# Optimization experiments

Hardware: AMD Instinct MI355X
Metric: run time of the kernel (lower is better)

## Reference

```python
import jax, jax.numpy as jnp
import numpy as np

HEADS = 16
D_MODEL = 1024
HEAD_DIM = D_MODEL // HEADS


def setup_inputs() -> dict:
    key = jax.random.key(0)
    ks = jax.random.split(key, 11)
    B, S = 4, 2048
    scale_in = 1.0 / np.sqrt(HEAD_DIM)
    scale_out = 1.0 / np.sqrt(D_MODEL)
    return {
        "values": jax.random.normal(ks[0], (B, S, D_MODEL), dtype=jnp.float32),
        "keys": jax.random.normal(ks[1], (B, S, D_MODEL), dtype=jnp.float32),
        "query": jax.random.normal(ks[2], (B, S, D_MODEL), dtype=jnp.float32),
        "wq": jax.random.normal(ks[3], (HEAD_DIM, HEAD_DIM), dtype=jnp.float32) * scale_in,
        "bq": jax.random.normal(ks[4], (HEAD_DIM,), dtype=jnp.float32) * 0.01,
        "wk": jax.random.normal(ks[5], (HEAD_DIM, HEAD_DIM), dtype=jnp.float32) * scale_in,
        "bk": jax.random.normal(ks[6], (HEAD_DIM,), dtype=jnp.float32) * 0.01,
        "wv": jax.random.normal(ks[7], (HEAD_DIM, HEAD_DIM), dtype=jnp.float32) * scale_in,
        "bv": jax.random.normal(ks[8], (HEAD_DIM,), dtype=jnp.float32) * 0.01,
        "wo": jax.random.normal(ks[9], (D_MODEL, D_MODEL), dtype=jnp.float32) * scale_out,
        "bo": jax.random.normal(ks[10], (D_MODEL,), dtype=jnp.float32) * 0.01,
    }


def reference(values, keys, query, wq, bq, wk, bk, wv, bv, wo, bo):
    B, Sq = query.shape[0], query.shape[1]
    Sk, Sv = keys.shape[1], values.shape[1]
    # reshape to (n, s, h, d); per-head linear shares one [d,d] weight across heads
    v = values.reshape(B, Sv, HEADS, HEAD_DIM) @ wv.T + bv
    k = keys.reshape(B, Sk, HEADS, HEAD_DIM) @ wk.T + bk
    q = query.reshape(B, Sq, HEADS, HEAD_DIM) @ wq.T + bq
    # scores scaled by sqrt(d_model) (as in original, NOT sqrt(head_dim))
    energy = jnp.einsum("nqhd,nkhd->nhqk", q, k)
    attn = jax.nn.softmax(energy / jnp.sqrt(jnp.float32(D_MODEL)), axis=-1)
    out = jnp.einsum("nhqk,nkhd->nqhd", attn, v).reshape(B, Sq, D_MODEL)
    return out @ wo.T + bo
```

## Files before the change

kernel.cpp:

```cpp
#include <hip/hip_runtime.h>

typedef unsigned short u16;
typedef short  bfrag  __attribute__((ext_vector_type(8), may_alias));
typedef unsigned long long ull_a __attribute__((may_alias));
typedef int    int_a  __attribute__((may_alias));
typedef int    i4_a   __attribute__((ext_vector_type(4), may_alias));
typedef float  f4_a   __attribute__((ext_vector_type(4), may_alias));
typedef unsigned u32x2 __attribute__((ext_vector_type(2)));
typedef __attribute__((ext_vector_type(4)))  float facc4;
typedef __attribute__((ext_vector_type(16))) float facc16;

#define SEQ   2048
#define NHEAD 16
#define HD    64
#define DM    1024
#define BH    64
#define NTOK  8192
#define QSC   0.04508422f

#if defined(__has_builtin)
#if __has_builtin(__builtin_amdgcn_cvt_pk_bf16_f32)
#define HAS_CVT_PK 1
#endif
#if __has_builtin(__builtin_amdgcn_permlane32_swap)
#define HAS_PLSWAP 1
#endif
#endif
#ifndef HAS_CVT_PK
#define HAS_CVT_PK 0
#endif
#ifndef HAS_PLSWAP
#define HAS_PLSWAP 0
#endif

__device__ __forceinline__ u16 f2bf(float f){
  union { float f; unsigned u; } x; x.f = f;
  unsigned r = x.u + 0x7FFFu + ((x.u >> 16) & 1u);
  return (u16)(r >> 16);
}
__device__ __forceinline__ unsigned pk2(float a, float b){
#if HAS_CVT_PK
  auto r = __builtin_amdgcn_cvt_pk_bf16_f32(a, b);
  union { decltype(r) v; unsigned u; } x; x.v = r; return x.u;
#else
  return (unsigned)f2bf(a) | ((unsigned)f2bf(b) << 16);
#endif
}
__device__ __forceinline__ unsigned long long pk4(float a, float b, float c, float d){
  return (unsigned long long)pk2(a,b) | ((unsigned long long)pk2(c,d) << 32);
}
__device__ __forceinline__ void swap32(unsigned &a, unsigned &b){
#if HAS_PLSWAP
  u32x2 r = __builtin_amdgcn_permlane32_swap(a, b, false, false);
  a = r[0]; b = r[1];
#else
  int lane = threadIdx.x & 63; int hh = lane >> 5;
  unsigned pa = (unsigned)__shfl_xor((int)a, 32, 64);
  unsigned pb = (unsigned)__shfl_xor((int)b, 32, 64);
  unsigned na = hh ? pb : a;
  unsigned nb = hh ? b  : pa;
  a = na; b = nb;
#endif
}
__device__ __forceinline__ bfrag ld8f(const float* p){
  f4_a a = *(const f4_a*)p;
  f4_a b = *(const f4_a*)(p + 4);
  union { bfrag v; unsigned u[4]; } r;
  r.u[0] = pk2(a[0],a[1]); r.u[1] = pk2(a[2],a[3]);
  r.u[2] = pk2(b[0],b[1]); r.u[3] = pk2(b[2],b[3]);
  return r.v;
}
__device__ __forceinline__ void stage16(const u16* g, u16* l){
  __builtin_amdgcn_global_load_lds((const __attribute__((address_space(1))) void*)g,
                                   (__attribute__((address_space(3))) void*)l, 16, 0, 0);
}

__global__ __launch_bounds__(256) void k_wconv(
  const float* __restrict__ wo, const float* __restrict__ wq,
  const float* __restrict__ wk, const float* __restrict__ wv,
  u16* __restrict__ dst)
{
  long i = ((long)blockIdx.x * 256 + threadIdx.x) * 8;
  const float* src; long off;
  if      (i < 1048576)        { src = wo; off = i; }
  else if (i < 1048576+4096)   { src = wq; off = i - 1048576; }
  else if (i < 1048576+8192)   { src = wk; off = i - (1048576+4096); }
  else                         { src = wv; off = i - (1048576+8192); }
  f4_a a = *(const f4_a*)(src + off);
  f4_a b = *(const f4_a*)(src + off + 4);
  ull_a* p = (ull_a*)(dst + i);
  p[0] = pk4(a[0],a[1],a[2],a[3]);
  p[1] = pk4(b[0],b[1],b[2],b[3]);
}

__global__ __launch_bounds__(256) void k_proj(
  const float* __restrict__ vin, const float* __restrict__ kin, const float* __restrict__ qin,
  const u16* __restrict__ wqb, const u16* __restrict__ wkb, const u16* __restrict__ wvb,
  const float* __restrict__ bq, const float* __restrict__ bk, const float* __restrict__ bv,
  u16* __restrict__ qo, u16* __restrict__ ko, u16* __restrict__ vo)
{
  __shared__ __align__(16) u16 Lq[16*264], Lk[16*264], Lv[16*264];
  int tid  = threadIdx.x;
  int wid  = tid >> 6, lane = tid & 63;
  int quad = lane >> 4, col = lane & 15;
  int token = blockIdx.x * 4 + wid;
  int b  = (blockIdx.x * 4) >> 11;
  int s0 = (blockIdx.x * 4) & 2047;
  long xbase = (long)token * DM;

  bfrag aq[2], ak[2], av[2];
  #pragma unroll
  for (int ks = 0; ks < 2; ks++){
    long off = xbase + (long)col * HD + ks*32 + quad*8;
    aq[ks] = ld8f(qin + off);
    ak[ks] = ld8f(kin + off);
    av[ks] = ld8f(vin + off);
  }
  #pragma unroll
  for (int ns = 0; ns < 4; ns++){
    facc4 accq = {0.f,0.f,0.f,0.f}, acck = {0.f,0.f,0.f,0.f}, accv = {0.f,0.f,0.f,0.f};
    #pragma unroll
    for (int ks = 0; ks < 2; ks++){
      int woff = (ns*16 + col) * HD + ks*32 + quad*8;
      bfrag bwq = *(const bfrag*)(wqb + woff);
      bfrag bwk = *(const bfrag*)(wkb + woff);
      bfrag bwv = *(const bfrag*)(wvb + woff);
      accq = __builtin_amdgcn_mfma_f32_16x16x32_bf16(aq[ks], bwq, accq, 0,0,0);
      acck = __builtin_amdgcn_mfma_f32_16x16x32_bf16(ak[ks], bwk, acck, 0,0,0);
      accv = __builtin_amdgcn_mfma_f32_16x16x32_bf16(av[ks], bwv, accv, 0,0,0);
    }
    int d = ns*16 + col;
    float fbq = bq[d], fbk = bk[d], fbv = bv[d];
    #pragma unroll
    for (int r = 0; r < 4; r++){
      int h = quad*4 + r;
      int li = h*264 + wid*64 + d;
      Lq[li] = f2bf((accq[r] + fbq) * QSC);
      Lk[li] = f2bf(acck[r] + fbk);
      Lv[li] = f2bf(accv[r] + fbv);
    }
  }
  __syncthreads();
  int h = tid >> 4, c = tid & 15;
  int src = h*264 + c*16;
  long gb = ((long)(b*NHEAD + h) * SEQ + s0) * HD + c*16;
  *(i4_a*)(qo + gb)     = *(const i4_a*)&Lq[src];
  *(i4_a*)(qo + gb + 8) = *(const i4_a*)&Lq[src + 8];
  *(i4_a*)(ko + gb)     = *(const i4_a*)&Lk[src];
  *(i4_a*)(ko + gb + 8) = *(const i4_a*)&Lk[src + 8];
  *(i4_a*)(vo + gb)     = *(const i4_a*)&Lv[src];
  *(i4_a*)(vo + gb + 8) = *(const i4_a*)&Lv[src + 8];
}

__global__ __launch_bounds__(256) void k_vtrans(
  const u16* __restrict__ vin, u16* __restrict__ vt)
{
  __shared__ __align__(16) u16 T[64*264];
  int tid = threadIdx.x;
  int wid = tid >> 6, lane = tid & 63;
  int s0  = blockIdx.x * 256;
  int bh  = blockIdx.y;
  const u16* ip = vin + ((long)bh * SEQ + s0 + tid) * HD;
  #pragma unroll
  for (int j = 0; j < 8; j++){
    bfrag v8 = *(const bfrag*)(ip + j*8);
    #pragma unroll
    for (int i = 0; i < 8; i++)
      T[(j*8 + i)*264 + tid] = (u16)((short*)&v8)[i];
  }
  __syncthreads();
  long obase = (long)bh * HD * SEQ + s0;
  #pragma unroll
  for (int it = 0; it < 16; it++){
    int d = it*4 + wid;
    ull_a v = *(const ull_a*)&T[d*264 + lane*4];
    *(ull_a*)(vt + obase + (long)d * SEQ + lane*4) = v;
  }
}

__global__ __launch_bounds__(512, 4) void k_attn(
  const u16* __restrict__ qws, const u16* __restrict__ kws, const u16* __restrict__ vt,
  u16* __restrict__ aout)
{
  __shared__ __align__(16) u16 KV[2][2][64*64];
  int tid = threadIdx.x;
  int wid = tid >> 6, lane = tid & 63;
  int ln = lane & 31, hh = lane >> 5;
  int bid = blockIdx.x;
  int xcd = bid & 7, lix = bid >> 3;
  int bh = xcd * 8 + (lix >> 3);
  int q0 = (lix & 7) * 256 + wid * 32;
  long base = (long)bh * SEQ * HD;

  int srow   = lane >> 3;
  int schunk = (lane & 7) ^ srow;

  bfrag qf[4];
  #pragma unroll
  for (int ks = 0; ks < 4; ks++)
    qf[ks] = *(const bfrag*)(qws + base + (long)(q0 + ln)*HD + ks*16 + hh*8);

  facc16 OO0, OO1;
  #pragma unroll
  for (int r = 0; r < 16; r++){ OO0[r] = 0.f; OO1[r] = 0.f; }
  float l_ = 0.f;

  stage16(kws + base + (long)(wid*8 + srow)*HD + schunk*8,  &KV[0][0][wid*512]);
  stage16(vt  + base + (long)(wid*8 + srow)*SEQ + schunk*8, &KV[0][1][wid*512]);

  auto tile = [&](int buf, int kt){
    __syncthreads();
    if (kt + 1 < 32){
      int k0n = (kt + 1) * 64;
      stage16(kws + base + (long)(k0n + wid*8 + srow)*HD + schunk*8, &KV[buf^1][0][wid*512]);
      stage16(vt  + base + (long)(wid*8 + srow)*SEQ + k0n + schunk*8, &KV[buf^1][1][wid*512]);
    }

    facc16 E0, E1;
    #pragma unroll
    for (int r = 0; r < 16; r++){ E0[r] = 0.f; E1[r] = 0.f; }
    __builtin_amdgcn_s_setprio(1);
    #pragma unroll
    for (int ks = 0; ks < 4; ks++){
      int sw = ((2*ks + hh) ^ (ln & 7)) * 8;
      bfrag kf0 = *(const bfrag*)&KV[buf][0][ ln      *64 + sw];
      bfrag kf1 = *(const bfrag*)&KV[buf][0][(32 + ln)*64 + sw];
      E0 = __builtin_amdgcn_mfma_f32_32x32x16_bf16(kf0, qf[ks], E0, 0,0,0);
      E1 = __builtin_amdgcn_mfma_f32_32x32x16_bf16(kf1, qf[ks], E1, 0,0,0);
    }
    __builtin_amdgcn_s_setprio(0);

    float rs = 0.f;
    #pragma unroll
    for (int r = 0; r < 16; r++){
      float p0 = __builtin_amdgcn_exp2f(E0[r]);
      float p1 = __builtin_amdgcn_exp2f(E1[r]);
      E0[r] = p0; E1[r] = p1; rs += p0 + p1;
    }
    l_ += rs;

    bfrag pf[4];
    #pragma unroll
    for (int half = 0; half < 2; half++){
      const facc16& P = half ? E1 : E0;
      #pragma unroll
      for (int k2 = 0; k2 < 2; k2++){
        int rb = k2 * 8;
        unsigned A0 = pk2(P[rb+0], P[rb+1]);
        unsigned A1 = pk2(P[rb+2], P[rb+3]);
        unsigned B0 = pk2(P[rb+4], P[rb+5]);
        unsigned B1 = pk2(P[rb+6], P[rb+7]);
        swap32(A0, B0);
        swap32(A1, B1);
        union { bfrag v; unsigned u[4]; } t;
        t.u[0] = A0; t.u[1] = A1; t.u[2] = B0; t.u[3] = B1;
        pf[half*2 + k2] = t.v;
      }
    }

    __builtin_amdgcn_s_setprio(1);
    #pragma unroll
    for (int ks = 0; ks < 4; ks++){
      int sw = ((2*ks + hh) ^ (ln & 7)) * 8;
      bfrag vf0 = *(const bfrag*)&KV[buf][1][ ln      *64 + sw];
      bfrag vf1 = *(const bfrag*)&KV[buf][1][(32 + ln)*64 + sw];
      OO0 = __builtin_amdgcn_mfma_f32_32x32x16_bf16(vf0, pf[ks], OO0, 0,0,0);
      OO1 = __builtin_amdgcn_mfma_f32_32x32x16_bf16(vf1, pf[ks], OO1, 0,0,0);
    }
    __builtin_amdgcn_s_setprio(0);
  };

  for (int kt = 0; kt < 32; kt += 2){
    tile(0, kt);
    tile(1, kt + 1);
  }

  l_ += __shfl_xor(l_, 32, 64);
  float inv = 1.0f / l_;
  int b_ = bh >> 4, h_ = bh & 15;
  long orow = ((long)(b_ * SEQ + q0 + ln) * NHEAD + h_) * HD;
  #pragma unroll
  for (int g = 0; g < 4; g++){
    *(ull_a*)(aout + orow +      8*g + 4*hh) =
      pk4(OO0[4*g]*inv, OO0[4*g+1]*inv, OO0[4*g+2]*inv, OO0[4*g+3]*inv);
    *(ull_a*)(aout + orow + 32 + 8*g + 4*hh) =
      pk4(OO1[4*g]*inv, OO1[4*g+1]*inv, OO1[4*g+2]*inv, OO1[4*g+3]*inv);
  }
}

__global__ __launch_bounds__(256) void k_oproj(
  const u16* __restrict__ A, const u16* __restrict__ Bw,
  const float* __restrict__ bo, float* __restrict__ out)
{
  __shared__ __align__(16) u16 As[128*64];
  __shared__ __align__(16) u16 Bs[128*64];
  int tid  = threadIdx.x;
  int wid  = tid >> 6, lane = tid & 63;
  int quad = lane >> 4, col = lane & 15;
  int m0 = blockIdx.x * 128;
  int n0 = blockIdx.y * 128;
  int wm = (wid & 1) * 64, wn = (wid >> 1) * 64;

  facc4 acc[4][4];
  #pragma unroll
  for (int i = 0; i < 4; i++)
    #pragma unroll
    for (int j = 0; j < 4; j++) acc[i][j] = {0.f,0.f,0.f,0.f};

  int srow = wid*8 + (lane >> 3);
  int scol = (lane & 7) * 8;
  const u16* Ag = A  + (long)(m0 + srow) * DM + scol;
  const u16* Bg = Bw + (long)(n0 + srow) * DM + scol;

  for (int k0 = 0; k0 < DM; k0 += 64){
    __syncthreads();
    #pragma unroll
    for (int j = 0; j < 4; j++){
      stage16(Ag + (long)j*32*DM + k0, &As[(j*32 + wid*8)*64]);
      stage16(Bg + (long)j*32*DM + k0, &Bs[(j*32 + wid*8)*64]);
    }
    __syncthreads();

    #pragma unroll
    for (int ks = 0; ks < 2; ks++){
      bfrag af[4], bf[4];
      #pragma unroll
      for (int i = 0; i < 4; i++)
        af[i] = *(const bfrag*)&As[(wm + i*16 + col)*64 + ks*32 + quad*8];
      #pragma unroll
      for (int i = 0; i < 4; i++)
        bf[i] = *(const bfrag*)&Bs[(wn + i*16 + col)*64 + ks*32 + quad*8];
      #pragma unroll
      for (int i = 0; i < 4; i++)
        #pragma unroll
        for (int j = 0; j < 4; j++)
          acc[i][j] = __builtin_amdgcn_mfma_f32_16x16x32_bf16(af[i], bf[j], acc[i][j], 0,0,0);
    }
  }

  #pragma unroll
  for (int j = 0; j < 4; j++){
    int n = n0 + wn + j*16 + col;
    float bias = bo[n];
    #pragma unroll
    for (int i = 0; i < 4; i++){
      long mrow = m0 + wm + i*16 + quad*4;
      #pragma unroll
      for (int r = 0; r < 4; r++)
        out[(mrow + r) * DM + n] = acc[i][j][r] + bias;
    }
  }
}

extern "C" void kernel_launch(void* const* d_in, const int* in_sizes, int n_in,
                              void* d_out, int out_size, void* d_ws, size_t ws_size,
                              hipStream_t stream)
{
  const float* values = (const float*)d_in[0];
  const float* keys   = (const float*)d_in[1];
  const float* query  = (const float*)d_in[2];
  const float* wq = (const float*)d_in[3];
  const float* bq = (const float*)d_in[4];
  const float* wk = (const float*)d_in[5];
  const float* bk = (const float*)d_in[6];
  const float* wv = (const float*)d_in[7];
  const float* bv = (const float*)d_in[8];
  const float* wo = (const float*)d_in[9];
  const float* bo = (const float*)d_in[10];

  const long N = 8388608;
  u16* qws  = (u16*)d_ws;
  u16* kws  = qws  + N;
  u16* vws  = kws  + N;
  u16* vtws = vws  + N;
  u16* wob  = vtws + N;
  u16* wqb  = wob + 1048576;
  u16* wkb  = wqb + 4096;
  u16* wvb  = wkb + 4096;
  u16* aws  = vws;

  k_wconv <<<518,           256, 0, stream>>>(wo, wq, wk, wv, wob);
  k_proj  <<<2048,          256, 0, stream>>>(values, keys, query, wqb, wkb, wvb,
                                              bq, bk, bv, qws, kws, vws);
  k_vtrans<<<dim3(8, 64),   256, 0, stream>>>(vws, vtws);
  k_attn  <<<512,           512, 0, stream>>>(qws, kws, vtws, aws);
  k_oproj <<<dim3(64, 8),   256, 0, stream>>>(aws, wob, bo, (float*)d_out);
}
```

Baseline: 307.0 us.

## Fuse V transpose into QKV projection and restructure per-head projection tiling

The projection kernel now runs one block per (128-token tile, head) and uses 32x32x16 MFMAs with the fp32 weights converted to bf16 inline, so the separate weight-conversion step for wq/wk/wv goes away. V is written straight into the transposed layout the attention kernel reads, which removes the k_vtrans launch and its extra global round trip. Q and K are staged through a small shared tile so they can be written out coalesced. The risk is that the transposed V stores are 2-byte scattered writes with a stride of SEQ, and each block reloads and reconverts the weight matrices.

```diff
diff --git a/kernel.cpp b/kernel.cpp
--- a/kernel.cpp
+++ b/kernel.cpp
@@ -76,105 +76,117 @@
 }
 
 __global__ __launch_bounds__(256) void k_wconv(
-  const float* __restrict__ wo, const float* __restrict__ wq,
-  const float* __restrict__ wk, const float* __restrict__ wv,
-  u16* __restrict__ dst)
+  const float* __restrict__ wo, u16* __restrict__ dst)
 {
   long i = ((long)blockIdx.x * 256 + threadIdx.x) * 8;
-  const float* src; long off;
-  if      (i < 1048576)        { src = wo; off = i; }
-  else if (i < 1048576+4096)   { src = wq; off = i - 1048576; }
-  else if (i < 1048576+8192)   { src = wk; off = i - (1048576+4096); }
-  else                         { src = wv; off = i - (1048576+8192); }
-  f4_a a = *(const f4_a*)(src + off);
-  f4_a b = *(const f4_a*)(src + off + 4);
+  f4_a a = *(const f4_a*)(wo + i);
+  f4_a b = *(const f4_a*)(wo + i + 4);
   ull_a* p = (ull_a*)(dst + i);
   p[0] = pk4(a[0],a[1],a[2],a[3]);
   p[1] = pk4(b[0],b[1],b[2],b[3]);
 }
 
-__global__ __launch_bounds__(256) void k_proj(
+__global__ __launch_bounds__(256, 4) void k_proj(
   const float* __restrict__ vin, const float* __restrict__ kin, const float* __restrict__ qin,
-  const u16* __restrict__ wqb, const u16* __restrict__ wkb, const u16* __restrict__ wvb,
+  const float* __restrict__ wq, const float* __restrict__ wk, const float* __restrict__ wv,
   const float* __restrict__ bq, const float* __restrict__ bk, const float* __restrict__ bv,
-  u16* __restrict__ qo, u16* __restrict__ ko, u16* __restrict__ vo)
-{
-  __shared__ __align__(16) u16 Lq[16*264], Lk[16*264], Lv[16*264];
-  int tid  = threadIdx.x;
-  int wid  = tid >> 6, lane = tid & 63;
-  int quad = lane >> 4, col = lane & 15;
-  int token = blockIdx.x * 4 + wid;
-  int b  = (blockIdx.x * 4) >> 11;
-  int s0 = (blockIdx.x * 4) & 2047;
-  long xbase = (long)token * DM;
-
-  bfrag aq[2], ak[2], av[2];
-  #pragma unroll
-  for (int ks = 0; ks < 2; ks++){
-    long off = xbase + (long)col * HD + ks*32 + quad*8;
-    aq[ks] = ld8f(qin + off);
-    ak[ks] = ld8f(kin + off);
-    av[ks] = ld8f(vin + off);
-  }
-  #pragma unroll
-  for (int ns = 0; ns < 4; ns++){
-    facc4 accq = {0.f,0.f,0.f,0.f}, acck = {0.f,0.f,0.f,0.f}, accv = {0.f,0.f,0.f,0.f};
-    #pragma unroll
-    for (int ks = 0; ks < 2; ks++){
-      int woff = (ns*16 + col) * HD + ks*32 + quad*8;
-      bfrag bwq = *(const bfrag*)(wqb + woff);
-      bfrag bwk = *(const bfrag*)(wkb + woff);
-      bfrag bwv = *(const bfrag*)(wvb + woff);
-      accq = __builtin_amdgcn_mfma_f32_16x16x32_bf16(aq[ks], bwq, accq, 0,0,0);
-      acck = __builtin_amdgcn_mfma_f32_16x16x32_bf16(ak[ks], bwk, acck, 0,0,0);
-      accv = __builtin_amdgcn_mfma_f32_16x16x32_bf16(av[ks], bwv, accv, 0,0,0);
-    }
-    int d = ns*16 + col;
-    float fbq = bq[d], fbk = bk[d], fbv = bv[d];
-    #pragma unroll
-    for (int r = 0; r < 4; r++){
-      int h = quad*4 + r;
-      int li = h*264 + wid*64 + d;
-      Lq[li] = f2bf((accq[r] + fbq) * QSC);
-      Lk[li] = f2bf(acck[r] + fbk);
-      Lv[li] = f2bf(accv[r] + fbv);
-    }
-  }
-  __syncthreads();
-  int h = tid >> 4, c = tid & 15;
-  int src = h*264 + c*16;
-  long gb = ((long)(b*NHEAD + h) * SEQ + s0) * HD + c*16;
-  *(i4_a*)(qo + gb)     = *(const i4_a*)&Lq[src];
-  *(i4_a*)(qo + gb + 8) = *(const i4_a*)&Lq[src + 8];
-  *(i4_a*)(ko + gb)     = *(const i4_a*)&Lk[src];
-  *(i4_a*)(ko + gb + 8) = *(const i4_a*)&Lk[src + 8];
-  *(i4_a*)(vo + gb)     = *(const i4_a*)&Lv[src];
-  *(i4_a*)(vo + gb + 8) = *(const i4_a*)&Lv[src + 8];
-}
-
-__global__ __launch_bounds__(256) void k_vtrans(
-  const u16* __restrict__ vin, u16* __restrict__ vt)
-{
-  __shared__ __align__(16) u16 T[64*264];
+  u16* __restrict__ qo, u16* __restrict__ ko, u16* __restrict__ vt)
+{
+  __shared__ __align__(16) u16 LT[128*68];
   int tid = threadIdx.x;
   int wid = tid >> 6, lane = tid & 63;
-  int s0  = blockIdx.x * 256;
-  int bh  = blockIdx.y;
-  const u16* ip = vin + ((long)bh * SEQ + s0 + tid) * HD;
-  #pragma unroll
-  for (int j = 0; j < 8; j++){
-    bfrag v8 = *(const bfrag*)(ip + j*8);
-    #pragma unroll
-    for (int i = 0; i < 8; i++)
-      T[(j*8 + i)*264 + tid] = (u16)((short*)&v8)[i];
+  int ln = lane & 31, hh = lane >> 5;
+  int h  = blockIdx.y;
+  int t0 = blockIdx.x * 128;
+  int b  = t0 >> 11;
+  int s0 = t0 & 2047;
+  int bh = b * NHEAD + h;
+  int tok = t0 + wid*32 + ln;
+  long xoff = (long)tok * DM + h * HD;
+
+  auto run_mm = [&](const float* __restrict__ x, const float* __restrict__ w,
+                    facc16* acc){
+    bfrag bx[4], aw[2][4];
+    #pragma unroll
+    for (int ks = 0; ks < 4; ks++)
+      bx[ks] = ld8f(x + xoff + ks*16 + hh*8);
+    #pragma unroll
+    for (int dt = 0; dt < 2; dt++)
+      #pragma unroll
+      for (int ks = 0; ks < 4; ks++)
+        aw[dt][ks] = ld8f(w + (dt*32 + ln)*HD + ks*16 + hh*8);
+    #pragma unroll
+    for (int dt = 0; dt < 2; dt++){
+      facc16 a;
+      #pragma unroll
+      for (int r = 0; r < 16; r++) a[r] = 0.f;
+      #pragma unroll
+      for (int ks = 0; ks < 4; ks++)
+        a = __builtin_amdgcn_mfma_f32_32x32x16_bf16(aw[dt][ks], bx[ks], a, 0,0,0);
+      acc[dt] = a;
+    }
+  };
+
+  {
+    facc16 acc[2]; run_mm(vin, wv, acc);
+    int s = s0 + wid*32 + ln;
+    long vb = (long)bh * HD * SEQ + s;
+    #pragma unroll
+    for (int dt = 0; dt < 2; dt++)
+      #pragma unroll
+      for (int g = 0; g < 4; g++){
+        f4_a bb = *(const f4_a*)(bv + dt*32 + g*8 + 4*hh);
+        #pragma unroll
+        for (int j = 0; j < 4; j++){
+          int d = dt*32 + g*8 + 4*hh + j;
+          vt[vb + (long)d * SEQ] = f2bf(acc[dt][g*4+j] + bb[j]);
+        }
+      }
+  }
+
+  {
+    facc16 acc[2]; run_mm(qin, wq, acc);
+    int row = wid*32 + ln;
+    #pragma unroll
+    for (int dt = 0; dt < 2; dt++)
+      #pragma unroll
+      for (int g = 0; g < 4; g++){
+        f4_a bb = *(const f4_a*)(bq + dt*32 + g*8 + 4*hh);
+        *(ull_a*)&LT[row*68 + dt*32 + g*8 + 4*hh] =
+          pk4((acc[dt][g*4+0]+bb[0])*QSC, (acc[dt][g*4+1]+bb[1])*QSC,
+              (acc[dt][g*4+2]+bb[2])*QSC, (acc[dt][g*4+3]+bb[3])*QSC);
+      }
   }
   __syncthreads();
-  long obase = (long)bh * HD * SEQ + s0;
-  #pragma unroll
-  for (int it = 0; it < 16; it++){
-    int d = it*4 + wid;
-    ull_a v = *(const ull_a*)&T[d*264 + lane*4];
-    *(ull_a*)(vt + obase + (long)d * SEQ + lane*4) = v;
+  {
+    int rr = tid >> 1, half = tid & 1;
+    long gb = ((long)bh * SEQ + s0 + rr) * HD + half*32;
+    #pragma unroll
+    for (int j = 0; j < 4; j++)
+      *(i4_a*)(qo + gb + j*8) = *(const i4_a*)&LT[rr*68 + half*32 + j*8];
+  }
+  __syncthreads();
+
+  {
+    facc16 acc[2]; run_mm(kin, wk, acc);
+    int row = wid*32 + ln;
+    #pragma unroll
+    for (int dt = 0; dt < 2; dt++)
+      #pragma unroll
+      for (int g = 0; g < 4; g++){
+        f4_a bb = *(const f4_a*)(bk + dt*32 + g*8 + 4*hh);
+        *(ull_a*)&LT[row*68 + dt*32 + g*8 + 4*hh] =
+          pk4(acc[dt][g*4+0]+bb[0], acc[dt][g*4+1]+bb[1],
+              acc[dt][g*4+2]+bb[2], acc[dt][g*4+3]+bb[3]);
+      }
+  }
+  __syncthreads();
+  {
+    int rr = tid >> 1, half = tid & 1;
+    long gb = ((long)bh * SEQ + s0 + rr) * HD + half*32;
+    #pragma unroll
+    for (int j = 0; j < 4; j++)
+      *(i4_a*)(ko + gb + j*8) = *(const i4_a*)&LT[rr*68 + half*32 + j*8];
   }
 }
 
@@ -374,15 +386,11 @@
   u16* vws  = kws  + N;
   u16* vtws = vws  + N;
   u16* wob  = vtws + N;
-  u16* wqb  = wob + 1048576;
-  u16* wkb  = wqb + 4096;
-  u16* wvb  = wkb + 4096;
   u16* aws  = vws;
 
-  k_wconv <<<518,           256, 0, stream>>>(wo, wq, wk, wv, wob);
-  k_proj  <<<2048,          256, 0, stream>>>(values, keys, query, wqb, wkb, wvb,
-                                              bq, bk, bv, qws, kws, vws);
-  k_vtrans<<<dim3(8, 64),   256, 0, stream>>>(vws, vtws);
+  k_wconv <<<512,           256, 0, stream>>>(wo, wob);
+  k_proj  <<<dim3(64, 16),  256, 0, stream>>>(values, keys, query, wq, wk, wv,
+                                              bq, bk, bv, qws, kws, vtws);
   k_attn  <<<512,           512, 0, stream>>>(qws, kws, vtws, aws);
   k_oproj <<<dim3(64, 8),   256, 0, stream>>>(aws, wob, bo, (float*)d_out);
 }
```

Result: faster. 288.3 us (-6.1%).
